# Kernel tuning notes

Measured on AMD Instinct MI355X. Metric: run time of the kernel, lower is better.

Reference implementation:

```python
import jax, jax.numpy as jnp
import numpy as np

DIM = 64  # module-level global `dim` used as the softmax scale


def setup_inputs() -> dict:
    key = jax.random.key(0)
    kq, kk, kv, km = jax.random.split(key, 4)
    B, H, S, d = 4, 16, 2048, DIM
    Q = jax.random.normal(kq, (B, H, S, d), dtype=jnp.float32)
    K = jax.random.normal(kk, (B, H, S, d), dtype=jnp.float32)
    V = jax.random.normal(kv, (B, H, S, d), dtype=jnp.float32)
    attn_mask = jax.random.randint(km, (B, H, S, S), 0, 2).astype(jnp.bool_)
    return {"Q": Q, "K": K, "V": V, "attn_mask": attn_mask}


def reference(Q, K, V, attn_mask):
    scale = 1.0 / np.sqrt(DIM).astype(np.float32)
    # scores: [B, H, S, S]
    scores = jnp.einsum("bhqd,bhkd->bhqk", Q, K) * scale
    # NOTE: original torch code does masked_fill_(attn_mask, 0) — fills with 0, not -inf
    scores = jnp.where(attn_mask, jnp.zeros((), scores.dtype), scores)
    attn = jax.nn.softmax(scores, axis=-1)
    context = jnp.einsum("bhqk,bhkd->bhqd", attn, V)
    return context
```

## Files before the change

### kernel.cpp

```cpp
#include <hip/hip_runtime.h>
#include <hip/hip_bf16.h>

typedef __bf16 bf16;
typedef __attribute__((ext_vector_type(8))) __bf16 bf16x8;
typedef __attribute__((ext_vector_type(4))) __bf16 bf16x4;
typedef __attribute__((ext_vector_type(4))) float f32x4;
typedef __attribute__((ext_vector_type(4))) int i32x4;

constexpr int SLEN = 2048;
constexpr int DH = 64;
constexpr int NBH = 64;
constexpr float SCALE_LOG2E = 0.125f * 1.4426950408889634f;

__global__ __launch_bounds__(256) void prep_kv_kernel(
    const float* __restrict__ K, const float* __restrict__ V,
    bf16* __restrict__ Kb, bf16* __restrict__ Vt)
{
    __shared__ float t[64][65];
    const int bh = blockIdx.y;
    const int s0 = blockIdx.x * 64;
    const int tx = threadIdx.x & 63, ty = threadIdx.x >> 6;

    const float* vp = V + ((size_t)bh * SLEN + s0) * DH;
    #pragma unroll
    for (int r = ty; r < 64; r += 4) t[r][tx] = vp[(size_t)r * DH + tx];

    {
        const float* kp = K + ((size_t)bh * SLEN + s0) * DH;
        bf16* kbp = Kb + ((size_t)bh * SLEN + s0) * DH;
        int r = threadIdx.x >> 2, c = (threadIdx.x & 3) * 16;
        const float4* src = (const float4*)(kp + (size_t)r * DH + c);
        float4 a = src[0], b = src[1], c2 = src[2], d = src[3];
        bf16x8 o0, o1;
        o0[0]=(bf16)a.x;  o0[1]=(bf16)a.y;  o0[2]=(bf16)a.z;  o0[3]=(bf16)a.w;
        o0[4]=(bf16)b.x;  o0[5]=(bf16)b.y;  o0[6]=(bf16)b.z;  o0[7]=(bf16)b.w;
        o1[0]=(bf16)c2.x; o1[1]=(bf16)c2.y; o1[2]=(bf16)c2.z; o1[3]=(bf16)c2.w;
        o1[4]=(bf16)d.x;  o1[5]=(bf16)d.y;  o1[6]=(bf16)d.z;  o1[7]=(bf16)d.w;
        *(bf16x8*)(kbp + (size_t)r * DH + c)     = o0;
        *(bf16x8*)(kbp + (size_t)r * DH + c + 8) = o1;
    }

    __syncthreads();
    bf16* op = Vt + (size_t)bh * DH * SLEN + s0;
    #pragma unroll
    for (int r = ty; r < 64; r += 4) op[(size_t)r * SLEN + tx] = (bf16)t[tx][r];
}

__device__ __forceinline__ void gl_lds16(const void* g, void* l) {
    __builtin_amdgcn_global_load_lds(
        (const __attribute__((address_space(1))) void*)g,
        (__attribute__((address_space(3))) void*)l, 16, 0, 0);
}

__global__ __launch_bounds__(256, 4) void attn_kernel(
    const float* __restrict__ Q, const int* __restrict__ mask,
    const bf16* __restrict__ Kb, const bf16* __restrict__ Vtb,
    float* __restrict__ out)
{
    __shared__ char KT[2][8192];
    __shared__ char VT[2][8192];
    __shared__ char PT[8192];

    const int h = blockIdx.x;
    const int logical = (h & 7) * 256 + (h >> 3);
    const int bh = logical >> 5;
    const int qbase = (logical & 31) * 64;
    const int tid = threadIdx.x;
    const int w = tid >> 6, l = tid & 63;
    const int lq = l & 15, lg = l >> 4;

    const char* kgb = (const char*)(Kb + (size_t)bh * SLEN * DH);
    const char* vgb = (const char*)(Vtb + (size_t)bh * DH * SLEN);

    const int kv_r = l >> 3;
    const int kv_c = ((l & 7) * 16) ^ (kv_r << 4);

    bf16x8 aq[2];
    {
        const float* qp = Q + ((size_t)bh * SLEN + qbase + w * 16 + lq) * DH + lg * 8;
        #pragma unroll
        for (int t = 0; t < 2; ++t) {
            float4 x = *(const float4*)(qp + t * 32);
            float4 y = *(const float4*)(qp + t * 32 + 4);
            bf16x8 f;
            f[0]=(bf16)x.x; f[1]=(bf16)x.y; f[2]=(bf16)x.z; f[3]=(bf16)x.w;
            f[4]=(bf16)y.x; f[5]=(bf16)y.y; f[6]=(bf16)y.z; f[7]=(bf16)y.w;
            aq[t] = f;
        }
    }

    f32x4 acc[4] = {{0,0,0,0},{0,0,0,0},{0,0,0,0},{0,0,0,0}};
    float dpart = 0.f;
    const int swzk = (lq & 7) << 4;
    const int prow = w * 16 + lq;
    char* pb = PT + prow * 128;
    const int pswz = (prow & 7) << 4;

    const int* mrow = mask + ((size_t)bh * SLEN + qbase + w * 16 + lq) * SLEN;

    auto stage = [&](int t, int buf) {
        const int kb = t * 64;
        #pragma unroll
        for (int q = 0; q < 2; ++q) {
            int r = (w * 2 + q) * 8 + kv_r;
            gl_lds16(kgb + (size_t)(kb + r) * 128 + kv_c, &KT[buf][(w * 2 + q) * 1024]);
            gl_lds16(vgb + (size_t)r * 4096 + (size_t)kb * 2 + kv_c, &VT[buf][(w * 2 + q) * 1024]);
        }
    };
    auto loadmask = [&](int t, i32x4* m) {
        #pragma unroll
        for (int n = 0; n < 4; ++n)
            m[n] = __builtin_nontemporal_load((const i32x4*)(mrow + t * 64 + n * 16 + lg * 4));
    };
    auto body = [&](int cur, const i32x4* mC) {
        #pragma unroll
        for (int n = 0; n < 4; ++n) {
            f32x4 s = {0, 0, 0, 0};
            #pragma unroll
            for (int t = 0; t < 2; ++t) {
                bf16x8 bk = *(const bf16x8*)&KT[cur][(n * 16 + lq) * 128 + ((t * 64 + lg * 16) ^ swzk)];
                s = __builtin_amdgcn_mfma_f32_16x16x32_bf16(bk, aq[t], s, 0, 0, 0);
            }
            bf16x4 pk;
            #pragma unroll
            for (int i = 0; i < 4; ++i) {
                float e = mC[n][i] ? 0.0f : s[i] * SCALE_LOG2E;
                float p = exp2f(e);
                dpart += p;
                pk[i] = (bf16)p;
            }
            *(bf16x4*)(pb + ((n * 32 + lg * 8) ^ pswz)) = pk;
        }
        #pragma unroll
        for (int n = 0; n < 4; ++n) {
            #pragma unroll
            for (int kk = 0; kk < 2; ++kk) {
                bf16x8 ap = *(const bf16x8*)(pb + ((kk * 64 + lg * 16) ^ pswz));
                bf16x8 bv = *(const bf16x8*)&VT[cur][(n * 16 + lq) * 128 + ((kk * 64 + lg * 16) ^ swzk)];
                acc[n] = __builtin_amdgcn_mfma_f32_16x16x32_bf16(ap, bv, acc[n], 0, 0, 0);
            }
        }
    };
    auto tile_sync = [&]() {
        asm volatile("s_waitcnt vmcnt(4) lgkmcnt(0)" ::: "memory");
        __builtin_amdgcn_s_barrier();
        __builtin_amdgcn_sched_barrier(0);
    };

    i32x4 mA[4], mB[4];

    stage(0, 0);
    __builtin_amdgcn_sched_barrier(0);
    loadmask(0, mA);
    tile_sync();

    for (int kt = 0; kt < SLEN / 64; kt += 2) {
        stage(kt + 1, 1);
        __builtin_amdgcn_sched_barrier(0);
        loadmask(kt + 1, mB);
        body(0, mA);
        tile_sync();

        const bool more = (kt + 2) < (SLEN / 64);
        if (more) {
            stage(kt + 2, 0);
            __builtin_amdgcn_sched_barrier(0);
            loadmask(kt + 2, mA);
        }
        body(1, mB);
        if (more) tile_sync();
    }

    dpart += __shfl_xor(dpart, 16, 64);
    dpart += __shfl_xor(dpart, 32, 64);
    float dinv = 1.0f / dpart;

    float di[4];
    #pragma unroll
    for (int i = 0; i < 4; ++i) di[i] = __shfl(dinv, lg * 4 + i, 64);

    float* op = out + ((size_t)bh * SLEN + qbase + w * 16) * DH;
    #pragma unroll
    for (int n = 0; n < 4; ++n) {
        #pragma unroll
        for (int i = 0; i < 4; ++i)
            op[(size_t)(lg * 4 + i) * DH + n * 16 + lq] = acc[n][i] * di[i];
    }
}

extern "C" void kernel_launch(void* const* d_in, const int* in_sizes, int n_in,
                              void* d_out, int out_size, void* d_ws, size_t ws_size,
                              hipStream_t stream) {
    const float* Q    = (const float*)d_in[0];
    const float* K    = (const float*)d_in[1];
    const float* V    = (const float*)d_in[2];
    const int*   mask = (const int*)d_in[3];
    float* out = (float*)d_out;

    bf16* Kb  = (bf16*)d_ws;
    bf16* Vtb = Kb + (size_t)NBH * SLEN * DH;

    prep_kv_kernel<<<dim3(SLEN / 64, NBH), 256, 0, stream>>>(K, V, Kb, Vtb);
    attn_kernel<<<2048, 256, 0, stream>>>(Q, mask, Kb, Vtb, out);
}
```

Before: 312.3 us.

## Keep softmax probabilities in registers and use 16x16x16 MFMA for PV

Drops the LDS round-trip for the probability tile P: exponentiated scores stay in registers in the layout of the QK^T MFMA output and feed directly into 16x16x16 bf16 MFMAs for the P·V product. This removes LDS writes and reads of P and the 8 KB PT buffer, which may allow higher occupancy. In exchange it issues twice as many smaller MFMAs with narrower (8-byte) V loads from LDS, and an inline-asm fallback with hand-placed nops if the builtin is missing.

```diff
diff --git a/kernel.cpp b/kernel.cpp
--- a/kernel.cpp
+++ b/kernel.cpp
@@ -6,6 +6,7 @@
 typedef __attribute__((ext_vector_type(4))) __bf16 bf16x4;
 typedef __attribute__((ext_vector_type(4))) float f32x4;
 typedef __attribute__((ext_vector_type(4))) int i32x4;
+typedef __attribute__((ext_vector_type(4))) short s16x4;
 
 constexpr int SLEN = 2048;
 constexpr int DH = 64;
@@ -52,6 +53,20 @@
         (__attribute__((address_space(3))) void*)l, 16, 0, 0);
 }
 
+__device__ __forceinline__ f32x4 pv_mfma(bf16x4 a, bf16x4 b, f32x4 c) {
+#if __has_builtin(__builtin_amdgcn_mfma_f32_16x16x16bf16_1k)
+    return __builtin_amdgcn_mfma_f32_16x16x16bf16_1k(
+        __builtin_bit_cast(s16x4, a), __builtin_bit_cast(s16x4, b), c, 0, 0, 0);
+#else
+    f32x4 d;
+    asm("s_nop 1\n\t"
+        "v_mfma_f32_16x16x16_bf16 %0, %1, %2, %3\n\t"
+        "s_nop 7"
+        : "=v"(d) : "v"(a), "v"(b), "v"(c));
+    return d;
+#endif
+}
+
 __global__ __launch_bounds__(256, 4) void attn_kernel(
     const float* __restrict__ Q, const int* __restrict__ mask,
     const bf16* __restrict__ Kb, const bf16* __restrict__ Vtb,
@@ -59,7 +74,6 @@
 {
     __shared__ char KT[2][8192];
     __shared__ char VT[2][8192];
-    __shared__ char PT[8192];
 
     const int h = blockIdx.x;
     const int logical = (h & 7) * 256 + (h >> 3);
@@ -92,9 +106,6 @@
     f32x4 acc[4] = {{0,0,0,0},{0,0,0,0},{0,0,0,0},{0,0,0,0}};
     float dpart = 0.f;
     const int swzk = (lq & 7) << 4;
-    const int prow = w * 16 + lq;
-    char* pb = PT + prow * 128;
-    const int pswz = (prow & 7) << 4;
 
     const int* mrow = mask + ((size_t)bh * SLEN + qbase + w * 16 + lq) * SLEN;
 
@@ -113,6 +124,7 @@
             m[n] = __builtin_nontemporal_load((const i32x4*)(mrow + t * 64 + n * 16 + lg * 4));
     };
     auto body = [&](int cur, const i32x4* mC) {
+        bf16x4 p[4];
         #pragma unroll
         for (int n = 0; n < 4; ++n) {
             f32x4 s = {0, 0, 0, 0};
@@ -121,23 +133,20 @@
                 bf16x8 bk = *(const bf16x8*)&KT[cur][(n * 16 + lq) * 128 + ((t * 64 + lg * 16) ^ swzk)];
                 s = __builtin_amdgcn_mfma_f32_16x16x32_bf16(bk, aq[t], s, 0, 0, 0);
             }
-            bf16x4 pk;
             #pragma unroll
             for (int i = 0; i < 4; ++i) {
                 float e = mC[n][i] ? 0.0f : s[i] * SCALE_LOG2E;
-                float p = exp2f(e);
-                dpart += p;
-                pk[i] = (bf16)p;
+                float pe = exp2f(e);
+                dpart += pe;
+                p[n][i] = (bf16)pe;
             }
-            *(bf16x4*)(pb + ((n * 32 + lg * 8) ^ pswz)) = pk;
-        }
-        #pragma unroll
-        for (int n = 0; n < 4; ++n) {
+        }
+        #pragma unroll
+        for (int nn = 0; nn < 4; ++nn) {
             #pragma unroll
-            for (int kk = 0; kk < 2; ++kk) {
-                bf16x8 ap = *(const bf16x8*)(pb + ((kk * 64 + lg * 16) ^ pswz));
-                bf16x8 bv = *(const bf16x8*)&VT[cur][(n * 16 + lq) * 128 + ((kk * 64 + lg * 16) ^ swzk)];
-                acc[n] = __builtin_amdgcn_mfma_f32_16x16x32_bf16(ap, bv, acc[n], 0, 0, 0);
+            for (int n = 0; n < 4; ++n) {
+                bf16x4 bv = *(const bf16x4*)&VT[cur][(nn * 16 + lq) * 128 + ((n * 32 + lg * 8) ^ swzk)];
+                acc[nn] = pv_mfma(p[n], bv, acc[nn]);
             }
         }
     };
```

Measured after the change: 314.2 us. Within noise of the previous version (+0.6%).
